# Kernel optimization log

Measured on AMD Instinct MI355X. Metric: run time of the kernel, lower is better.

## Reference

```python
import jax, jax.numpy as jnp
import numpy as np

NUM_BLOCKS = 2
RES_LAYERS = 10
HID = 128
IN_CH = 256
MID_CH = 512
OUT_CH = 256
DILATIONS = [2 ** l for b in range(NUM_BLOCKS) for l in range(RES_LAYERS)]
GOOD = sum(DILATIONS)  # 2046
NLAYERS = NUM_BLOCKS * RES_LAYERS


def setup_inputs() -> dict:
    key = jax.random.key(0)
    ks = jax.random.split(key, 16)
    s = 0.05
    B, T = 8, 8192
    inp = {
        "inputs": jax.random.normal(ks[0], (B, IN_CH, T), dtype=jnp.float32),
        "Wi": jax.random.normal(ks[1], (HID, IN_CH), dtype=jnp.float32) * s,
        "bi": jax.random.normal(ks[2], (HID,), dtype=jnp.float32) * s,
        "Wf": jax.random.normal(ks[3], (NLAYERS, HID, HID, 2), dtype=jnp.float32) * s,
        "bf": jax.random.normal(ks[4], (NLAYERS, HID), dtype=jnp.float32) * s,
        "Wg": jax.random.normal(ks[5], (NLAYERS, HID, HID, 2), dtype=jnp.float32) * s,
        "bg": jax.random.normal(ks[6], (NLAYERS, HID), dtype=jnp.float32) * s,
        "Wr": jax.random.normal(ks[7], (NLAYERS, HID, HID), dtype=jnp.float32) * s,
        "br": jax.random.normal(ks[8], (NLAYERS, HID), dtype=jnp.float32) * s,
        "W1": jax.random.normal(ks[9], (MID_CH, HID), dtype=jnp.float32) * s,
        "b1": jax.random.normal(ks[10], (MID_CH,), dtype=jnp.float32) * s,
        "W2": jax.random.normal(ks[11], (OUT_CH, MID_CH), dtype=jnp.float32) * s,
        "b2": jax.random.normal(ks[12], (OUT_CH,), dtype=jnp.float32) * s,
    }
    return inp


def _dilated_k2(x, W, b, d):
    # x: [B, C, T] -> [B, C, T-d]
    y = jnp.einsum("oi,bit->bot", W[:, :, 0], x[:, :, :-d]) \
        + jnp.einsum("oi,bit->bot", W[:, :, 1], x[:, :, d:])
    return y + b[None, :, None]


def reference(inputs, Wi, bi, Wf, bf, Wg, bg, Wr, br, W1, b1, W2, b2):
    T = inputs.shape[2]
    target = T - GOOD
    res = jnp.einsum("oi,bit->bot", Wi, inputs) + bi[None, :, None]
    final = None
    for idx, d in enumerate(DILATIONS):
        f = jnp.tanh(_dilated_k2(res, Wf[idx], bf[idx], d))
        g = jax.nn.sigmoid(_dilated_k2(res, Wg[idx], bg[idx], d))
        out = f * g
        x = jnp.einsum("oi,bit->bot", Wr[idx], out) + br[idx][None, :, None]
        res = x + res[:, :, d:]
        # NOTE: original code computes split conv then immediately overwrites
        # it with x[:, :, -target:]; the split conv is dead code, so skip it.
        skip = x[:, :, -target:]
        final = skip if final is None else final + skip
    h = jax.nn.relu(final)
    h = jnp.einsum("oi,bit->bot", W1, h) + b1[None, :, None]
    h = jax.nn.relu(h)
    h = jnp.einsum("oi,bit->bot", W2, h) + b2[None, :, None]
    n, c, l = h.shape
    return jnp.transpose(h, (0, 2, 1)).reshape(n * l, c)
```

## Files before the change

kernel.cpp:

```cpp
#include <hip/hip_runtime.h>


#define TT 8192
#define HIDC 128
#define GOODC 2046
#define TGT 6146
#define NL 20

typedef _Float16 half8_t __attribute__((ext_vector_type(8)));
typedef _Float16 half4_t __attribute__((ext_vector_type(4)));
typedef float floatx4 __attribute__((ext_vector_type(4)));

__device__ __forceinline__ floatx4 mfma16(half8_t a, half8_t b, floatx4 c) {
  return __builtin_amdgcn_mfma_f32_16x16x32_f16(a, b, c, 0, 0, 0);
}

__global__ void prep_kernel(const float* __restrict__ Wi, const float* __restrict__ Wf,
                            const float* __restrict__ Wg, const float* __restrict__ Wr,
                            const float* __restrict__ W1, const float* __restrict__ W2,
                            _Float16* __restrict__ WIh, _Float16* __restrict__ WFG,
                            _Float16* __restrict__ WRh, _Float16* __restrict__ W1h,
                            _Float16* __restrict__ W2h) {
  int idx = blockIdx.x * blockDim.x + threadIdx.x;
  int stride = gridDim.x * blockDim.x;
  for (int i = idx; i < NL * 256 * 256; i += stride) {
    int l = i >> 16; int m = (i >> 8) & 255; int k = i & 255;
    int tap = k >> 7; int ci = k & 127;
    float v;
    if (m < 128) v = Wf[(((size_t)l * 128 + m) * 128 + ci) * 2 + tap];
    else         v = Wg[(((size_t)l * 128 + (m - 128)) * 128 + ci) * 2 + tap];
    WFG[i] = (_Float16)v;
  }
  for (int i = idx; i < NL * 128 * 128; i += stride) WRh[i] = (_Float16)Wr[i];
  for (int i = idx; i < 128 * 256; i += stride) WIh[i] = (_Float16)Wi[i];
  for (int i = idx; i < 512 * 128; i += stride) W1h[i] = (_Float16)W1[i];
  for (int i = idx; i < 256 * 512; i += stride) W2h[i] = (_Float16)W2[i];
}

__global__ __launch_bounds__(256, 3) void input_kernel(
    const float* __restrict__ inp, const _Float16* __restrict__ WIh,
    const float* __restrict__ bi, _Float16* __restrict__ R0) {
  __shared__ __align__(16) _Float16 Xs[64][264];
  const int tid = threadIdx.x;
  const int lane = tid & 63;
  const int w = tid >> 6;
  const int ml = lane & 15;
  const int mq = lane >> 4;
  const int b = blockIdx.y;
  const int u0 = blockIdx.x * 64;
  const float* ib = inp + (size_t)b * 256 * TT;

  for (int i = tid; i < 64 * 16; i += 256) {
    int n4 = i & 15;
    int kg = i >> 4;
    const float* src = ib + (size_t)(kg * 4) * TT + u0 + n4 * 4;
    floatx4 c0 = *(const floatx4*)(src);
    floatx4 c1 = *(const floatx4*)(src + TT);
    floatx4 c2 = *(const floatx4*)(src + 2 * TT);
    floatx4 c3 = *(const floatx4*)(src + 3 * TT);
#pragma unroll
    for (int t = 0; t < 4; ++t) {
      half4_t h;
      h[0] = (_Float16)c0[t]; h[1] = (_Float16)c1[t];
      h[2] = (_Float16)c2[t]; h[3] = (_Float16)c3[t];
      *(half4_t*)&Xs[n4 * 4 + t][kg * 4] = h;
    }
  }
  __syncthreads();

  floatx4 acc[2][4];
#pragma unroll
  for (int a = 0; a < 2; ++a)
#pragma unroll
    for (int c = 0; c < 4; ++c) acc[a][c] = floatx4{0.f, 0.f, 0.f, 0.f};

  const _Float16* Aw = WIh + (size_t)(32 * w + ml) * 256;
  for (int kk = 0; kk < 8; ++kk) {
    const int ko = kk * 32 + mq * 8;
    half8_t a0 = *(const half8_t*)(Aw + ko);
    half8_t a1 = *(const half8_t*)(Aw + 16 * 256 + ko);
#pragma unroll
    for (int nt = 0; nt < 4; ++nt) {
      half8_t bv = *(const half8_t*)&Xs[nt * 16 + ml][ko];
      acc[0][nt] = mfma16(a0, bv, acc[0][nt]);
      acc[1][nt] = mfma16(a1, bv, acc[1][nt]);
    }
  }
  __syncthreads();
  float* Xf = (float*)&Xs[0][0];
#pragma unroll
  for (int mt = 0; mt < 2; ++mt) {
    const int mb = 32 * w + mt * 16 + mq * 4;
#pragma unroll
    for (int nt = 0; nt < 4; ++nt)
      *(floatx4*)&Xf[(nt * 16 + ml) * 132 + mb] = acc[mt][nt];
  }
  __syncthreads();
  _Float16* Rb = R0 + (size_t)b * TT * HIDC;
  for (int i = tid; i < 64 * 16; i += 256) {
    int n = i >> 4; int c = i & 15;
    floatx4 x0 = *(const floatx4*)&Xf[n * 132 + c * 8];
    floatx4 x1 = *(const floatx4*)&Xf[n * 132 + c * 8 + 4];
    floatx4 b0 = *(const floatx4*)(bi + c * 8);
    floatx4 b1v = *(const floatx4*)(bi + c * 8 + 4);
    half8_t h;
#pragma unroll
    for (int t = 0; t < 4; ++t) {
      h[t] = (_Float16)(x0[t] + b0[t]);
      h[4 + t] = (_Float16)(x1[t] + b1v[t]);
    }
    *(half8_t*)(Rb + (size_t)(u0 + n) * HIDC + c * 8) = h;
  }
}

__global__ __launch_bounds__(512, 4) void layer_kernel(
    const _Float16* __restrict__ Rin, _Float16* __restrict__ Rout,
    const _Float16* __restrict__ WFG, const _Float16* __restrict__ WR,
    const float* __restrict__ bf, const float* __restrict__ bg,
    const float* __restrict__ br, int d, int ustart) {
  __shared__ __align__(16) _Float16 Xs[128][136];
  __shared__ __align__(16) _Float16 Os[128][136];
  const int tid = threadIdx.x;
  const int lane = tid & 63;
  const int w = tid >> 6;
  const int wm = w & 3;
  const int wn = w >> 2;
  const int ml = lane & 15;
  const int mq = lane >> 4;
  const int b = blockIdx.y;
  const int u0 = ustart + blockIdx.x * 128;
  const _Float16* Rb = Rin + (size_t)b * TT * HIDC;
  _Float16* Ro = Rout + (size_t)b * TT * HIDC;

  floatx4 accF[2][4], accG[2][4];
#pragma unroll
  for (int a = 0; a < 2; ++a)
#pragma unroll
    for (int c = 0; c < 4; ++c) {
      accF[a][c] = floatx4{0.f, 0.f, 0.f, 0.f};
      accG[a][c] = floatx4{0.f, 0.f, 0.f, 0.f};
    }

  for (int p = 0; p < 2; ++p) {
    for (int i = tid; i < 128 * 16; i += 512) {
      int n = i >> 4; int c = i & 15;
      int u = u0 + n - (p ? 0 : d);
      if (u > TT - 1) u = TT - 1;
      *(half8_t*)&Xs[n][c * 8] = *(const half8_t*)(Rb + (size_t)u * HIDC + c * 8);
    }
    __syncthreads();
    const _Float16* Af = WFG + (size_t)(32 * wm + ml) * 256 + p * 128;
    const _Float16* Ag = WFG + (size_t)(128 + 32 * wm + ml) * 256 + p * 128;
    for (int kk = 0; kk < 4; ++kk) {
      const int ko = kk * 32 + mq * 8;
      half8_t aF0 = *(const half8_t*)(Af + ko);
      half8_t aF1 = *(const half8_t*)(Af + 16 * 256 + ko);
      half8_t aG0 = *(const half8_t*)(Ag + ko);
      half8_t aG1 = *(const half8_t*)(Ag + 16 * 256 + ko);
#pragma unroll
      for (int nt = 0; nt < 4; ++nt) {
        half8_t bv = *(const half8_t*)&Xs[wn * 64 + nt * 16 + ml][ko];
        accF[0][nt] = mfma16(aF0, bv, accF[0][nt]);
        accF[1][nt] = mfma16(aF1, bv, accF[1][nt]);
        accG[0][nt] = mfma16(aG0, bv, accG[0][nt]);
        accG[1][nt] = mfma16(aG1, bv, accG[1][nt]);
      }
    }
    __syncthreads();
  }

#pragma unroll
  for (int mt = 0; mt < 2; ++mt) {
    const int mb = 32 * wm + mt * 16 + mq * 4;
    floatx4 bfv = *(const floatx4*)(bf + mb);
    floatx4 bgv = *(const floatx4*)(bg + mb);
#pragma unroll
    for (int nt = 0; nt < 4; ++nt) {
      half4_t o;
#pragma unroll
      for (int r = 0; r < 4; ++r) {
        float fp = accF[mt][nt][r] + bfv[r];
        float gp = accG[mt][nt][r] + bgv[r];
        float fv = 2.0f / (1.0f + __expf(-2.0f * fp)) - 1.0f;
        float gv = 1.0f / (1.0f + __expf(-gp));
        o[r] = (_Float16)(fv * gv);
      }
      *(half4_t*)&Os[wn * 64 + nt * 16 + ml][mb] = o;
    }
  }
  __syncthreads();

  floatx4 accX[2][4];
#pragma unroll
  for (int a = 0; a < 2; ++a)
#pragma unroll
    for (int c = 0; c < 4; ++c) accX[a][c] = floatx4{0.f, 0.f, 0.f, 0.f};
  const _Float16* Ar = WR + (size_t)(32 * wm + ml) * 128;
#pragma unroll
  for (int kk = 0; kk < 4; ++kk) {
    const int ko = kk * 32 + mq * 8;
    half8_t a0 = *(const half8_t*)(Ar + ko);
    half8_t a1 = *(const half8_t*)(Ar + 16 * 128 + ko);
#pragma unroll
    for (int nt = 0; nt < 4; ++nt) {
      half8_t bv = *(const half8_t*)&Os[wn * 64 + nt * 16 + ml][ko];
      accX[0][nt] = mfma16(a0, bv, accX[0][nt]);
      accX[1][nt] = mfma16(a1, bv, accX[1][nt]);
    }
  }
  __syncthreads();

#pragma unroll
  for (int mt = 0; mt < 2; ++mt) {
    const int mb = 32 * wm + mt * 16 + mq * 4;
#pragma unroll
    for (int nt = 0; nt < 4; ++nt) {
      half4_t h;
#pragma unroll
      for (int r = 0; r < 4; ++r) h[r] = (_Float16)accX[mt][nt][r];
      *(half4_t*)&Os[wn * 64 + nt * 16 + ml][mb] = h;
    }
  }
  __syncthreads();

  for (int i = tid; i < 128 * 16; i += 512) {
    int n = i >> 4; int c = i & 15;
    int u = u0 + n;
    if (u < TT) {
      half8_t xv = *(const half8_t*)&Os[n][c * 8];
      half8_t rv = *(const half8_t*)&Xs[n][c * 8];
      floatx4 b0 = *(const floatx4*)(br + c * 8);
      floatx4 b1v = *(const floatx4*)(br + c * 8 + 4);
      half8_t o;
#pragma unroll
      for (int t = 0; t < 4; ++t) {
        o[t] = (_Float16)((float)xv[t] + (float)rv[t] + b0[t]);
        o[4 + t] = (_Float16)((float)xv[4 + t] + (float)rv[4 + t] + b1v[t]);
      }
      *(half8_t*)(Ro + (size_t)u * HIDC + c * 8) = o;
    }
  }
}

__global__ __launch_bounds__(512, 4) void head_kernel(
    const _Float16* __restrict__ Rfin, const _Float16* __restrict__ R0,
    const _Float16* __restrict__ W1h, const _Float16* __restrict__ W2h,
    const float* __restrict__ b1, const float* __restrict__ b2,
    float* __restrict__ out) {
  __shared__ __align__(16) _Float16 Hs[64][136];
  __shared__ __align__(16) _Float16 H1s[64][264];
  const int tid = threadIdx.x;
  const int lane = tid & 63;
  const int w = tid >> 6;
  const int ml = lane & 15;
  const int mq = lane >> 4;
  const int b = blockIdx.y;
  const int u0 = GOODC + blockIdx.x * 64;
  const _Float16* Ra = Rfin + (size_t)b * TT * HIDC;
  const _Float16* Rz = R0 + (size_t)b * TT * HIDC;

  for (int i = tid; i < 64 * 16; i += 512) {
    int n = i >> 4; int c = i & 15;
    int u = u0 + n; if (u > TT - 1) u = TT - 1;
    half8_t a = *(const half8_t*)(Ra + (size_t)u * HIDC + c * 8);
    half8_t z = *(const half8_t*)(Rz + (size_t)u * HIDC + c * 8);
    half8_t h;
#pragma unroll
    for (int t = 0; t < 8; ++t) {
      float v = (float)a[t] - (float)z[t];
      h[t] = (_Float16)(v > 0.f ? v : 0.f);
    }
    *(half8_t*)&Hs[n][c * 8] = h;
  }
  __syncthreads();

  floatx4 acc2[2][4];
#pragma unroll
  for (int a = 0; a < 2; ++a)
#pragma unroll
    for (int c = 0; c < 4; ++c) acc2[a][c] = floatx4{0.f, 0.f, 0.f, 0.f};

  for (int p = 0; p < 2; ++p) {
    floatx4 acc1[2][4];
#pragma unroll
    for (int a = 0; a < 2; ++a)
#pragma unroll
      for (int c = 0; c < 4; ++c) acc1[a][c] = floatx4{0.f, 0.f, 0.f, 0.f};
    const _Float16* A1 = W1h + (size_t)(256 * p + 32 * w + ml) * 128;
#pragma unroll
    for (int kk = 0; kk < 4; ++kk) {
      const int ko = kk * 32 + mq * 8;
      half8_t av0 = *(const half8_t*)(A1 + ko);
      half8_t av1 = *(const half8_t*)(A1 + 16 * 128 + ko);
#pragma unroll
      for (int nt = 0; nt < 4; ++nt) {
        half8_t bv = *(const half8_t*)&Hs[nt * 16 + ml][ko];
        acc1[0][nt] = mfma16(av0, bv, acc1[0][nt]);
        acc1[1][nt] = mfma16(av1, bv, acc1[1][nt]);
      }
    }
    __syncthreads();
#pragma unroll
    for (int mt = 0; mt < 2; ++mt) {
      const int mb = 32 * w + mt * 16 + mq * 4;
      floatx4 bv = *(const floatx4*)(b1 + 256 * p + mb);
#pragma unroll
      for (int nt = 0; nt < 4; ++nt) {
        half4_t h;
#pragma unroll
        for (int r = 0; r < 4; ++r) {
          float v = acc1[mt][nt][r] + bv[r];
          h[r] = (_Float16)(v > 0.f ? v : 0.f);
        }
        *(half4_t*)&H1s[nt * 16 + ml][mb] = h;
      }
    }
    __syncthreads();
    const _Float16* A2 = W2h + (size_t)(32 * w + ml) * 512 + p * 256;
    for (int kk = 0; kk < 8; ++kk) {
      const int ko = kk * 32 + mq * 8;
      half8_t av0 = *(const half8_t*)(A2 + ko);
      half8_t av1 = *(const half8_t*)(A2 + 16 * 512 + ko);
#pragma unroll
      for (int nt = 0; nt < 4; ++nt) {
        half8_t bv = *(const half8_t*)&H1s[nt * 16 + ml][ko];
        acc2[0][nt] = mfma16(av0, bv, acc2[0][nt]);
        acc2[1][nt] = mfma16(av1, bv, acc2[1][nt]);
      }
    }
    __syncthreads();
  }

#pragma unroll
  for (int mt = 0; mt < 2; ++mt) {
    const int mb = 32 * w + mt * 16 + mq * 4;
    floatx4 bv = *(const floatx4*)(b2 + mb);
#pragma unroll
    for (int nt = 0; nt < 4; ++nt) {
      half4_t h;
#pragma unroll
      for (int r = 0; r < 4; ++r) h[r] = (_Float16)(acc2[mt][nt][r] + bv[r]);
      *(half4_t*)&H1s[nt * 16 + ml][mb] = h;
    }
  }
  __syncthreads();
  for (int i = tid; i < 64 * 32; i += 512) {
    int n = i >> 5; int g = i & 31;
    int u = u0 + n;
    if (u < TT) {
      half8_t v = *(const half8_t*)&H1s[n][g * 8];
      float* dst = out + ((size_t)b * TGT + (u - GOODC)) * 256 + g * 8;
      floatx4 v0, v1;
#pragma unroll
      for (int t = 0; t < 4; ++t) { v0[t] = (float)v[t]; v1[t] = (float)v[4 + t]; }
      *(floatx4*)dst = v0;
      *(floatx4*)(dst + 4) = v1;
    }
  }
}

extern "C" void kernel_launch(void* const* d_in, const int* in_sizes, int n_in,
                              void* d_out, int out_size, void* d_ws, size_t ws_size,
                              hipStream_t stream) {
  const float* inputs = (const float*)d_in[0];
  const float* Wi = (const float*)d_in[1];
  const float* bi = (const float*)d_in[2];
  const float* Wf = (const float*)d_in[3];
  const float* bf = (const float*)d_in[4];
  const float* Wg = (const float*)d_in[5];
  const float* bg = (const float*)d_in[6];
  const float* Wr = (const float*)d_in[7];
  const float* br = (const float*)d_in[8];
  const float* W1 = (const float*)d_in[9];
  const float* b1 = (const float*)d_in[10];
  const float* W2 = (const float*)d_in[11];
  const float* b2 = (const float*)d_in[12];
  float* out = (float*)d_out;

  char* ws = (char*)d_ws;
  _Float16* R0h = (_Float16*)(ws + 0);
  _Float16* Ph  = (_Float16*)(ws + 16777216);
  _Float16* Qh  = (_Float16*)(ws + 33554432);
  _Float16* WFG = (_Float16*)(ws + 50331648);
  _Float16* WRh = (_Float16*)(ws + 52953088);
  _Float16* WIh = (_Float16*)(ws + 53608448);
  _Float16* W1h = (_Float16*)(ws + 53673984);
  _Float16* W2h = (_Float16*)(ws + 53805056);

  prep_kernel<<<dim3(512), dim3(256), 0, stream>>>(Wi, Wf, Wg, Wr, W1, W2,
                                                   WIh, WFG, WRh, W1h, W2h);
  input_kernel<<<dim3(TT / 64, 8), dim3(256), 0, stream>>>(inputs, WIh, bi, R0h);

  int S = 0;
  for (int l = 0; l < NL; ++l) {
    int d = 1 << (l % 10);
    int ustart = S + d;
    const _Float16* rin = (l == 0) ? R0h : ((l & 1) ? Ph : Qh);
    _Float16* rout = (l & 1) ? Qh : Ph;
    int Lout = TT - ustart;
    int nblk = (Lout + 127) / 128;
    layer_kernel<<<dim3(nblk, 8), dim3(512), 0, stream>>>(
        rin, rout, WFG + (size_t)l * 65536, WRh + (size_t)l * 16384,
        bf + l * 128, bg + l * 128, br + l * 128, d, ustart);
    S = ustart;
  }
  head_kernel<<<dim3((TGT + 63) / 64, 8), dim3(512), 0, stream>>>(
      Qh, R0h, W1h, W2h, b1, b2, out);
}
```

Before: 857.5 us.

## Shrink layer tile to 96, load both taps upfront, fuse residual add

The layer kernel now uses a 96-column tile and loads both dilation taps into two shared buffers in a single phase, which removes the per-tap reload and its barrier. It raises the occupancy hint to 6 blocks. The residual add and bias are folded into the accumulator epilogue, so the final store becomes a plain copy. Tanh and sigmoid switch to hardware reciprocal. The smaller tile means more blocks and less weight reuse per block, and rcp gives a slightly less accurate result.

```diff
diff --git a/kernel.cpp b/kernel.cpp
--- a/kernel.cpp
+++ b/kernel.cpp
@@ -13,6 +13,13 @@
 
 __device__ __forceinline__ floatx4 mfma16(half8_t a, half8_t b, floatx4 c) {
   return __builtin_amdgcn_mfma_f32_16x16x32_f16(a, b, c, 0, 0, 0);
+}
+
+__device__ __forceinline__ float fast_sigmoid(float x) {
+  return __builtin_amdgcn_rcpf(1.0f + __expf(-x));
+}
+__device__ __forceinline__ float fast_tanh(float x) {
+  return 2.0f * __builtin_amdgcn_rcpf(1.0f + __expf(-2.0f * x)) - 1.0f;
 }
 
 __global__ void prep_kernel(const float* __restrict__ Wi, const float* __restrict__ Wf,
@@ -113,13 +120,13 @@
   }
 }
 
-__global__ __launch_bounds__(512, 4) void layer_kernel(
+__global__ __launch_bounds__(512, 6) void layer_kernel(
     const _Float16* __restrict__ Rin, _Float16* __restrict__ Rout,
     const _Float16* __restrict__ WFG, const _Float16* __restrict__ WR,
     const float* __restrict__ bf, const float* __restrict__ bg,
     const float* __restrict__ br, int d, int ustart) {
-  __shared__ __align__(16) _Float16 Xs[128][136];
-  __shared__ __align__(16) _Float16 Os[128][136];
+  __shared__ __align__(16) _Float16 Xs0[96][136];
+  __shared__ __align__(16) _Float16 Xs1[96][136];
   const int tid = threadIdx.x;
   const int lane = tid & 63;
   const int w = tid >> 6;
@@ -128,73 +135,85 @@
   const int ml = lane & 15;
   const int mq = lane >> 4;
   const int b = blockIdx.y;
-  const int u0 = ustart + blockIdx.x * 128;
+  const int u0 = ustart + blockIdx.x * 96;
   const _Float16* Rb = Rin + (size_t)b * TT * HIDC;
   _Float16* Ro = Rout + (size_t)b * TT * HIDC;
 
-  floatx4 accF[2][4], accG[2][4];
+#pragma unroll
+  for (int it = 0; it < 3; ++it) {
+    int j = it * 512 + tid;
+    int n = j >> 4, c = j & 15;
+    int ua = min(u0 + n - d, TT - 1);
+    int ub = min(u0 + n, TT - 1);
+    *(half8_t*)&Xs0[n][c * 8] = *(const half8_t*)(Rb + (size_t)ua * HIDC + c * 8);
+    *(half8_t*)&Xs1[n][c * 8] = *(const half8_t*)(Rb + (size_t)ub * HIDC + c * 8);
+  }
+  __syncthreads();
+
+  floatx4 accF[2][3], accG[2][3];
 #pragma unroll
   for (int a = 0; a < 2; ++a)
 #pragma unroll
-    for (int c = 0; c < 4; ++c) {
+    for (int c = 0; c < 3; ++c) {
       accF[a][c] = floatx4{0.f, 0.f, 0.f, 0.f};
       accG[a][c] = floatx4{0.f, 0.f, 0.f, 0.f};
     }
-
-  for (int p = 0; p < 2; ++p) {
-    for (int i = tid; i < 128 * 16; i += 512) {
-      int n = i >> 4; int c = i & 15;
-      int u = u0 + n - (p ? 0 : d);
-      if (u > TT - 1) u = TT - 1;
-      *(half8_t*)&Xs[n][c * 8] = *(const half8_t*)(Rb + (size_t)u * HIDC + c * 8);
-    }
-    __syncthreads();
-    const _Float16* Af = WFG + (size_t)(32 * wm + ml) * 256 + p * 128;
-    const _Float16* Ag = WFG + (size_t)(128 + 32 * wm + ml) * 256 + p * 128;
+  const _Float16* Af = WFG + (size_t)(32 * wm + ml) * 256;
+  const _Float16* Ag = Af + 128 * 256;
+#pragma unroll
+  for (int h = 0; h < 2; ++h) {
+    const _Float16(*X)[136] = h ? Xs1 : Xs0;
     for (int kk = 0; kk < 4; ++kk) {
       const int ko = kk * 32 + mq * 8;
-      half8_t aF0 = *(const half8_t*)(Af + ko);
-      half8_t aF1 = *(const half8_t*)(Af + 16 * 256 + ko);
-      half8_t aG0 = *(const half8_t*)(Ag + ko);
-      half8_t aG1 = *(const half8_t*)(Ag + 16 * 256 + ko);
-#pragma unroll
-      for (int nt = 0; nt < 4; ++nt) {
-        half8_t bv = *(const half8_t*)&Xs[wn * 64 + nt * 16 + ml][ko];
+      const int kw = h * 128 + ko;
+      half8_t aF0 = *(const half8_t*)(Af + kw);
+      half8_t aF1 = *(const half8_t*)(Af + 16 * 256 + kw);
+      half8_t aG0 = *(const half8_t*)(Ag + kw);
+      half8_t aG1 = *(const half8_t*)(Ag + 16 * 256 + kw);
+#pragma unroll
+      for (int nt = 0; nt < 3; ++nt) {
+        half8_t bv = *(const half8_t*)&X[wn * 48 + nt * 16 + ml][ko];
         accF[0][nt] = mfma16(aF0, bv, accF[0][nt]);
         accF[1][nt] = mfma16(aF1, bv, accF[1][nt]);
         accG[0][nt] = mfma16(aG0, bv, accG[0][nt]);
         accG[1][nt] = mfma16(aG1, bv, accG[1][nt]);
       }
     }
-    __syncthreads();
-  }
-
+  }
+
+  half4_t og[2][3];
 #pragma unroll
   for (int mt = 0; mt < 2; ++mt) {
     const int mb = 32 * wm + mt * 16 + mq * 4;
     floatx4 bfv = *(const floatx4*)(bf + mb);
     floatx4 bgv = *(const floatx4*)(bg + mb);
 #pragma unroll
-    for (int nt = 0; nt < 4; ++nt) {
-      half4_t o;
+    for (int nt = 0; nt < 3; ++nt) {
 #pragma unroll
       for (int r = 0; r < 4; ++r) {
-        float fp = accF[mt][nt][r] + bfv[r];
-        float gp = accG[mt][nt][r] + bgv[r];
-        float fv = 2.0f / (1.0f + __expf(-2.0f * fp)) - 1.0f;
-        float gv = 1.0f / (1.0f + __expf(-gp));
-        o[r] = (_Float16)(fv * gv);
+        float fv = fast_tanh(accF[mt][nt][r] + bfv[r]);
+        float gv = fast_sigmoid(accG[mt][nt][r] + bgv[r]);
+        og[mt][nt][r] = (_Float16)(fv * gv);
       }
-      *(half4_t*)&Os[wn * 64 + nt * 16 + ml][mb] = o;
-    }
-  }
-  __syncthreads();
-
-  floatx4 accX[2][4];
+    }
+  }
+  __syncthreads();
+
+  _Float16(*Os)[136] = Xs0;
+#pragma unroll
+  for (int mt = 0; mt < 2; ++mt) {
+    const int mb = 32 * wm + mt * 16 + mq * 4;
+#pragma unroll
+    for (int nt = 0; nt < 3; ++nt)
+      *(half4_t*)&Os[wn * 48 + nt * 16 + ml][mb] = og[mt][nt];
+  }
+  __syncthreads();
+
+  floatx4 accX[2][3];
 #pragma unroll
   for (int a = 0; a < 2; ++a)
 #pragma unroll
-    for (int c = 0; c < 4; ++c) accX[a][c] = floatx4{0.f, 0.f, 0.f, 0.f};
+    for (int c = 0; c < 3; ++c) accX[a][c] = floatx4{0.f, 0.f, 0.f, 0.f};
   const _Float16* Ar = WR + (size_t)(32 * wm + ml) * 128;
 #pragma unroll
   for (int kk = 0; kk < 4; ++kk) {
@@ -202,43 +221,45 @@
     half8_t a0 = *(const half8_t*)(Ar + ko);
     half8_t a1 = *(const half8_t*)(Ar + 16 * 128 + ko);
 #pragma unroll
-    for (int nt = 0; nt < 4; ++nt) {
-      half8_t bv = *(const half8_t*)&Os[wn * 64 + nt * 16 + ml][ko];
+    for (int nt = 0; nt < 3; ++nt) {
+      half8_t bv = *(const half8_t*)&Os[wn * 48 + nt * 16 + ml][ko];
       accX[0][nt] = mfma16(a0, bv, accX[0][nt]);
       accX[1][nt] = mfma16(a1, bv, accX[1][nt]);
     }
   }
-  __syncthreads();
-
+
+  half4_t xo[2][3];
 #pragma unroll
   for (int mt = 0; mt < 2; ++mt) {
     const int mb = 32 * wm + mt * 16 + mq * 4;
-#pragma unroll
-    for (int nt = 0; nt < 4; ++nt) {
-      half4_t h;
-#pragma unroll
-      for (int r = 0; r < 4; ++r) h[r] = (_Float16)accX[mt][nt][r];
-      *(half4_t*)&Os[wn * 64 + nt * 16 + ml][mb] = h;
-    }
-  }
-  __syncthreads();
-
-  for (int i = tid; i < 128 * 16; i += 512) {
-    int n = i >> 4; int c = i & 15;
+    floatx4 brv = *(const floatx4*)(br + mb);
+#pragma unroll
+    for (int nt = 0; nt < 3; ++nt) {
+      const int n = wn * 48 + nt * 16 + ml;
+      half4_t rold = *(const half4_t*)&Xs1[n][mb];
+#pragma unroll
+      for (int r = 0; r < 4; ++r)
+        xo[mt][nt][r] = (_Float16)(accX[mt][nt][r] + brv[r] + (float)rold[r]);
+    }
+  }
+  __syncthreads();
+
+#pragma unroll
+  for (int mt = 0; mt < 2; ++mt) {
+    const int mb = 32 * wm + mt * 16 + mq * 4;
+#pragma unroll
+    for (int nt = 0; nt < 3; ++nt)
+      *(half4_t*)&Os[wn * 48 + nt * 16 + ml][mb] = xo[mt][nt];
+  }
+  __syncthreads();
+
+#pragma unroll
+  for (int it = 0; it < 3; ++it) {
+    int j = it * 512 + tid;
+    int n = j >> 4, c = j & 15;
     int u = u0 + n;
-    if (u < TT) {
-      half8_t xv = *(const half8_t*)&Os[n][c * 8];
-      half8_t rv = *(const half8_t*)&Xs[n][c * 8];
-      floatx4 b0 = *(const floatx4*)(br + c * 8);
-      floatx4 b1v = *(const floatx4*)(br + c * 8 + 4);
-      half8_t o;
-#pragma unroll
-      for (int t = 0; t < 4; ++t) {
-        o[t] = (_Float16)((float)xv[t] + (float)rv[t] + b0[t]);
-        o[4 + t] = (_Float16)((float)xv[4 + t] + (float)rv[4 + t] + b1v[t]);
-      }
-      *(half8_t*)(Ro + (size_t)u * HIDC + c * 8) = o;
-    }
+    if (u < TT)
+      *(half8_t*)(Ro + (size_t)u * HIDC + c * 8) = *(const half8_t*)&Os[n][c * 8];
   }
 }
 
@@ -397,8 +418,7 @@
     int ustart = S + d;
     const _Float16* rin = (l == 0) ? R0h : ((l & 1) ? Ph : Qh);
     _Float16* rout = (l & 1) ? Qh : Ph;
-    int Lout = TT - ustart;
-    int nblk = (Lout + 127) / 128;
+    int nblk = (TT - ustart + 95) / 96;
     layer_kernel<<<dim3(nblk, 8), dim3(512), 0, stream>>>(
         rin, rout, WFG + (size_t)l * 65536, WRh + (size_t)l * 16384,
         bf + l * 128, bg + l * 128, br + l * 128, d, ustart);
```

New measurement: 1.557 ms. 81.6% more time.
